# Performance work log

Measured on AMD Instinct MI355X. Metric: run time of the kernel, lower is better.

## Reference

```python
import jax, jax.numpy as jnp
import numpy as np

K = 50  # top-k causal instances (UC_MIL constructor)


def setup_inputs() -> dict:
    key = jax.random.key(0)
    k1, k2 = jax.random.split(key)
    X = jax.random.normal(k1, (8, 4096, 768), dtype=jnp.float32)
    # GCN layer weight: nn.Linear(768, 1, bias=False) -> weight shape (1, 768)
    W = jax.random.normal(k2, (1, 768), dtype=jnp.float32) * 0.02
    return {"X": X, "W": W}


def reference(X, W):
    # X: (B, N, D) bag of instance features; W: (1, D) GCN weight
    B, N, D = X.shape
    k = K

    # --- build_adjacency_matrix, batched ---
    Xc = X - X.mean(axis=1, keepdims=True)                      # center over instances
    cov = jnp.einsum('bnd,bmd->bnm', Xc, Xc)                    # (B, N, N)
    var = jnp.sqrt(jnp.sum(Xc * Xc, axis=-1, keepdims=True)) + 1e-6  # (B, N, 1)
    corr = cov / (var * jnp.swapaxes(var, 1, 2))                # var @ var.T
    A = jnp.abs(corr)
    dinv = jnp.sum(A, axis=-1) ** (-0.5)                        # (B, N)
    # D @ A @ D with diagonal D == row/col scaling (same math, no dense diag)
    A_norm = dinv[:, :, None] * A * dinv[:, None, :]

    # --- 1-layer GCN score: (A_norm @ (X W^T)).squeeze(-1) ---
    XW = jnp.einsum('bnd,d->bn', X, W[0])                       # (B, N)
    S = jnp.einsum('bnm,bm->bn', A_norm, XW)                    # (B, N)

    # --- top-k causal / non-causal split, vectorized over batch ---
    _, topk_idx = jax.lax.top_k(S, k)                           # (B, k)
    F_c = jnp.take_along_axis(X, topk_idx[:, :, None], axis=1)  # (B, k, D)

    # non-topk indices in ascending order (torch.arange(N)[mask] semantics)
    flag = jnp.zeros((B, N), dtype=jnp.int32)
    flag = flag.at[jnp.arange(B)[:, None], topk_idx].set(1)
    non_idx = jnp.argsort(flag, axis=1, stable=True)[:, : N - k]  # (B, N-k)
    F_nc = jnp.take_along_axis(X, non_idx[:, :, None], axis=1)    # (B, N-k, D)

    # NOTE: original code has a bug: topk_indices = torch.stack(F_i_c, 0),
    # i.e. the second output is the gathered features, not the indices.
    # We replicate that faithfully.
    return (S,
            F_c,
            F_c.mean(axis=1, keepdims=True),
            F_nc.mean(axis=1, keepdims=True))
```

## Files before the change

kernel.cpp:

```cpp
#include <hip/hip_runtime.h>
#include <stdint.h>

typedef unsigned short u16;
typedef short bf16x8 __attribute__((ext_vector_type(8)));
typedef float f32x4 __attribute__((ext_vector_type(4)));
typedef unsigned long long ull;

#define NB 8
#define NROW 4096
#define ND 768
#define NKB 24
#define NRB 32
#define KTILE 4096
#define NTRI 528
#define TOPK 50

#define CPART_OFF 0u
#define CSUM_OFF  786432u
#define MEAN_OFF  811008u
#define RV_OFF    835584u
#define XW_OFF    966656u
#define T_OFF     1097728u
#define U_OFF     1228800u
#define SMALL_TOTAL 1359872u
#define HI_OFF    ((size_t)SMALL_TOTAL)
#define LO_OFF    (HI_OFF + 50331648ull)
#define COV_OFF   (LO_OFF + 50331648ull)

static __device__ __forceinline__ u16 f2bf(float f) {
  uint32_t u = __float_as_uint(f);
  u += 0x7FFFu + ((u >> 16) & 1u);
  return (u16)(u >> 16);
}
static __device__ __forceinline__ float bf2f(u16 h) {
  return __uint_as_float(((uint32_t)h) << 16);
}

static __device__ __forceinline__ void gload_lds16(const char* g, char* l) {
  __builtin_amdgcn_global_load_lds(
      (const __attribute__((address_space(1))) uint32_t*)(const void*)g,
      (__attribute__((address_space(3))) uint32_t*)(void*)l, 16, 0, 0);
}

static __device__ __forceinline__ int tile_swz(int t) {
  return (t & 7) * 66 + (t >> 3);
}

__global__ __launch_bounds__(256)
void colsum1_kernel(const float* __restrict__ X, float* __restrict__ part) {
  const int nc = blockIdx.x;
  const int d  = threadIdx.x + blockIdx.y * 256;
  const int b  = blockIdx.z;
  const float* p = X + ((size_t)b * NROW + (size_t)nc * 128) * ND + d;
  float s = 0.f;
  for (int i = 0; i < 128; ++i) s += p[(size_t)i * ND];
  part[((size_t)b * 32 + nc) * ND + d] = s;
}

__global__ __launch_bounds__(256)
void colsum2_kernel(const float* __restrict__ part, float* __restrict__ csum,
                    float* __restrict__ mean) {
  const int d = threadIdx.x + blockIdx.x * 256;
  const int b = blockIdx.y;
  float s = 0.f;
  for (int i = 0; i < 32; ++i) s += part[((size_t)b * 32 + i) * ND + d];
  csum[(size_t)b * ND + d] = s;
  mean[(size_t)b * ND + d] = s * (1.0f / 4096.0f);
}

__global__ __launch_bounds__(128)
void rowstats_kernel(const float* __restrict__ X, const float* __restrict__ W,
                     const float* __restrict__ mean,
                     u16* __restrict__ hi, u16* __restrict__ lo,
                     float* __restrict__ rv, float* __restrict__ xw) {
  const int n  = blockIdx.x;
  const int gb = blockIdx.y;
  const int tid = threadIdx.x;
  const float* xr = X + ((size_t)gb * NROW + n) * ND;
  const float* mb = mean + (size_t)gb * ND;
  const int r = n & 127, rbk = n >> 7;
  float ssq = 0.f, sw = 0.f;
  if (tid < 96) {
    const int d0 = tid * 8;
    const float4 xa = *(const float4*)(xr + d0);
    const float4 xb = *(const float4*)(xr + d0 + 4);
    const float4 ma = *(const float4*)(mb + d0);
    const float4 mc = *(const float4*)(mb + d0 + 4);
    const float4 wa = *(const float4*)(W + d0);
    const float4 wb = *(const float4*)(W + d0 + 4);
    float x[8]  = {xa.x, xa.y, xa.z, xa.w, xb.x, xb.y, xb.z, xb.w};
    float mm[8] = {ma.x, ma.y, ma.z, ma.w, mc.x, mc.y, mc.z, mc.w};
    float ww[8] = {wa.x, wa.y, wa.z, wa.w, wb.x, wb.y, wb.z, wb.w};
    u16 hbits[8], lbits[8];
#pragma unroll
    for (int i = 0; i < 8; ++i) {
      float xc = x[i] - mm[i];
      ssq += xc * xc;
      sw  += x[i] * ww[i];
      u16 hb = f2bf(xc);
      float hf = bf2f(hb);
      u16 lb2 = f2bf(xc - hf);
      hbits[i] = hb; lbits[i] = lb2;
    }
    const int kb = d0 >> 5;
    const int kk = d0 & 31;
    const size_t tbyte = ((size_t)((gb * NRB + rbk) * NKB + kb)) * 8192
                       + (size_t)((r * 64 + kk * 2) ^ ((r & 7) << 4));
    uint4 hv, lv;
    hv.x = (uint32_t)hbits[0] | ((uint32_t)hbits[1] << 16);
    hv.y = (uint32_t)hbits[2] | ((uint32_t)hbits[3] << 16);
    hv.z = (uint32_t)hbits[4] | ((uint32_t)hbits[5] << 16);
    hv.w = (uint32_t)hbits[6] | ((uint32_t)hbits[7] << 16);
    lv.x = (uint32_t)lbits[0] | ((uint32_t)lbits[1] << 16);
    lv.y = (uint32_t)lbits[2] | ((uint32_t)lbits[3] << 16);
    lv.z = (uint32_t)lbits[4] | ((uint32_t)lbits[5] << 16);
    lv.w = (uint32_t)lbits[6] | ((uint32_t)lbits[7] << 16);
    *(uint4*)((char*)hi + tbyte) = hv;
    *(uint4*)((char*)lo + tbyte) = lv;
  }
#pragma unroll
  for (int m = 1; m < 64; m <<= 1) {
    ssq += __shfl_xor(ssq, m, 64);
    sw  += __shfl_xor(sw, m, 64);
  }
  __shared__ float sh[4];
  const int w = tid >> 6, lane = tid & 63;
  if (lane == 0) { sh[w * 2] = ssq; sh[w * 2 + 1] = sw; }
  __syncthreads();
  if (tid == 0) {
    float S = sh[0] + sh[2];
    float T = sh[1] + sh[3];
    const size_t i = (size_t)gb * NROW + n;
    rv[i] = 1.0f / (sqrtf(S) + 1e-6f);
    xw[i] = T;
  }
}

static __device__ __forceinline__ bf16x8 read_frag(const u16* sm, int r, int kbyte) {
  const int byte = (r * 64 + kbyte) ^ ((r & 7) << 4);
  return *(const bf16x8*)((const char*)sm + byte);
}

__global__ __launch_bounds__(256, 2)
void gemm_acc_kernel(const u16* __restrict__ hi, const u16* __restrict__ lo,
                     const float* __restrict__ coef, float* __restrict__ outacc,
                     float* __restrict__ covout) {
  const int gb = blockIdx.y;
  const int tsw = tile_swz(blockIdx.x);
  int trem = tsw;
  int rb = 0;
  while (trem >= NRB - rb) { trem -= NRB - rb; ++rb; }
  const int cb = rb + trem;

  __shared__ u16 sm[4 * KTILE];
  u16* aHi = sm;
  u16* bHi = sm + KTILE;
  u16* aLo = sm + 2 * KTILE;
  u16* bLo = sm + 3 * KTILE;

  const int tid = threadIdx.x;
  const int lane = tid & 63;
  const int wid = tid >> 6;
  const int wrow = wid >> 1, wcol = wid & 1;
  const int l15 = lane & 15, lg = lane >> 4;

  const char* hA = (const char*)(hi + (size_t)((gb * NRB + rb) * NKB) * KTILE);
  const char* hB = (const char*)(hi + (size_t)((gb * NRB + cb) * NKB) * KTILE);
  const char* lA = (const char*)(lo + (size_t)((gb * NRB + rb) * NKB) * KTILE);
  const char* lB = (const char*)(lo + (size_t)((gb * NRB + cb) * NKB) * KTILE);

  f32x4 acc[4][4];
#pragma unroll
  for (int i = 0; i < 4; ++i)
#pragma unroll
    for (int j = 0; j < 4; ++j) acc[i][j] = f32x4{0.f, 0.f, 0.f, 0.f};

  for (int kb = 0; kb < NKB; ++kb) {
    __syncthreads();
    const size_t kb8 = (size_t)kb * 8192;
#pragma unroll
    for (int it = 0; it < 2; ++it) {
      const int off = it * 4096 + tid * 16;
      gload_lds16(hA + kb8 + off, (char*)aHi + off);
      gload_lds16(hB + kb8 + off, (char*)bHi + off);
      gload_lds16(lA + kb8 + off, (char*)aLo + off);
      gload_lds16(lB + kb8 + off, (char*)bLo + off);
    }
    __syncthreads();

    bf16x8 ah[4], bh[4], al[4], bl[4];
#pragma unroll
    for (int i = 0; i < 4; ++i) {
      ah[i] = read_frag(aHi, wrow * 64 + i * 16 + l15, lg * 16);
      bh[i] = read_frag(bHi, wcol * 64 + i * 16 + l15, lg * 16);
      al[i] = read_frag(aLo, wrow * 64 + i * 16 + l15, lg * 16);
      bl[i] = read_frag(bLo, wcol * 64 + i * 16 + l15, lg * 16);
    }
#pragma unroll
    for (int mi = 0; mi < 4; ++mi)
#pragma unroll
      for (int ni = 0; ni < 4; ++ni) {
        acc[mi][ni] = __builtin_amdgcn_mfma_f32_16x16x32_bf16(ah[mi], bh[ni], acc[mi][ni], 0, 0, 0);
        acc[mi][ni] = __builtin_amdgcn_mfma_f32_16x16x32_bf16(ah[mi], bl[ni], acc[mi][ni], 0, 0, 0);
        acc[mi][ni] = __builtin_amdgcn_mfma_f32_16x16x32_bf16(al[mi], bh[ni], acc[mi][ni], 0, 0, 0);
      }
  }

  const float* cf = coef + (size_t)gb * NROW;
  float* oa = outacc + (size_t)gb * NROW;
  const int rbase = rb * 128 + wrow * 64;
  const int cbase = cb * 128 + wcol * 64;

  float* cv = covout + ((size_t)gb * NTRI + tsw) * 16384;
#pragma unroll
  for (int mi = 0; mi < 4; ++mi)
#pragma unroll
    for (int ni = 0; ni < 4; ++ni)
#pragma unroll
      for (int j = 0; j < 4; ++j)
        cv[(wrow * 64 + mi * 16 + lg * 4 + j) * 128 + wcol * 64 + ni * 16 + l15] =
            fabsf(acc[mi][ni][j]);

  float ccol[4];
#pragma unroll
  for (int ni = 0; ni < 4; ++ni) ccol[ni] = cf[cbase + ni * 16 + l15];

  float rs[4][4];
#pragma unroll
  for (int mi = 0; mi < 4; ++mi)
#pragma unroll
    for (int j = 0; j < 4; ++j) {
      float s = 0.f;
#pragma unroll
      for (int ni = 0; ni < 4; ++ni) s += fabsf(acc[mi][ni][j]) * ccol[ni];
      rs[mi][j] = s;
    }
#pragma unroll
  for (int m = 1; m < 16; m <<= 1)
#pragma unroll
    for (int mi = 0; mi < 4; ++mi)
#pragma unroll
      for (int j = 0; j < 4; ++j) rs[mi][j] += __shfl_xor(rs[mi][j], m, 64);
  if (l15 == 0) {
#pragma unroll
    for (int mi = 0; mi < 4; ++mi)
#pragma unroll
      for (int j = 0; j < 4; ++j)
        atomicAdd(&oa[rbase + mi * 16 + lg * 4 + j], rs[mi][j]);
  }

  if (rb != cb) {
    float crow[4][4];
#pragma unroll
    for (int mi = 0; mi < 4; ++mi)
#pragma unroll
      for (int j = 0; j < 4; ++j) crow[mi][j] = cf[rbase + mi * 16 + lg * 4 + j];
    float cs[4];
#pragma unroll
    for (int ni = 0; ni < 4; ++ni) {
      float s = 0.f;
#pragma unroll
      for (int mi = 0; mi < 4; ++mi)
#pragma unroll
        for (int j = 0; j < 4; ++j) s += fabsf(acc[mi][ni][j]) * crow[mi][j];
      cs[ni] = s;
    }
#pragma unroll
    for (int ni = 0; ni < 4; ++ni) {
      cs[ni] += __shfl_xor(cs[ni], 16, 64);
      cs[ni] += __shfl_xor(cs[ni], 32, 64);
    }
    if (lg == 0) {
#pragma unroll
      for (int ni = 0; ni < 4; ++ni)
        atomicAdd(&oa[cbase + ni * 16 + l15], cs[ni]);
    }
  }
}

__global__ __launch_bounds__(256, 2)
void upass_kernel(const float* __restrict__ cov, const float* __restrict__ tt,
                  const float* __restrict__ rv, const float* __restrict__ xw,
                  float* __restrict__ uacc) {
  const int gb = blockIdx.y;
  const int tsw = tile_swz(blockIdx.x);
  int trem = tsw;
  int rb = 0;
  while (trem >= NRB - rb) { trem -= NRB - rb; ++rb; }
  const int cb = rb + trem;

  const float* A = cov + ((size_t)gb * NTRI + tsw) * 16384;
  const size_t bo = (size_t)gb * NROW;

  __shared__ float wr[128];
  __shared__ float plds[128 * 33];
  __shared__ float csum_p[8][128];

  const int t = threadIdx.x;
  const int g = t >> 5;
  const int l = t & 31;

  if (t < 128) {
    const int row = rb * 128 + t;
    wr[t] = (1.0f / sqrtf(rv[bo + row] * tt[bo + row])) * xw[bo + row] * rv[bo + row];
  }
  float4 wc4;
  {
    const int col = cb * 128 + l * 4;
    const float4 r4 = *(const float4*)(rv + bo + col);
    const float4 t4 = *(const float4*)(tt + bo + col);
    const float4 x4 = *(const float4*)(xw + bo + col);
    wc4.x = (1.0f / sqrtf(r4.x * t4.x)) * x4.x * r4.x;
    wc4.y = (1.0f / sqrtf(r4.y * t4.y)) * x4.y * r4.y;
    wc4.z = (1.0f / sqrtf(r4.z * t4.z)) * x4.z * r4.z;
    wc4.w = (1.0f / sqrtf(r4.w * t4.w)) * x4.w * r4.w;
  }
  __syncthreads();

  float sc0 = 0.f, sc1 = 0.f, sc2 = 0.f, sc3 = 0.f;
#pragma unroll
  for (int i = 0; i < 16; ++i) {
    const int r = g + i * 8;
    const f32x4 v = __builtin_nontemporal_load((const f32x4*)(A + r * 128 + l * 4));
    plds[r * 33 + l] = v[0] * wc4.x + v[1] * wc4.y + v[2] * wc4.z + v[3] * wc4.w;
    const float wrr = wr[r];
    sc0 += v[0] * wrr; sc1 += v[1] * wrr; sc2 += v[2] * wrr; sc3 += v[3] * wrr;
  }
  csum_p[g][l * 4 + 0] = sc0;
  csum_p[g][l * 4 + 1] = sc1;
  csum_p[g][l * 4 + 2] = sc2;
  csum_p[g][l * 4 + 3] = sc3;
  __syncthreads();

  float* ua = uacc + bo;
  if (t < 128) {
    float rsum = 0.f;
#pragma unroll
    for (int i = 0; i < 32; ++i) rsum += plds[t * 33 + i];
    atomicAdd(&ua[rb * 128 + t], rsum);
    if (rb != cb) {
      float s = 0.f;
#pragma unroll
      for (int gg = 0; gg < 8; ++gg) s += csum_p[gg][t];
      atomicAdd(&ua[cb * 128 + t], s);
    }
  }
}

__global__ __launch_bounds__(1024)
void topk_kernel(const float* __restrict__ tt, const float* __restrict__ rv,
                 const float* __restrict__ u, const float* __restrict__ X,
                 const float* __restrict__ csum, float* __restrict__ S,
                 float* __restrict__ outFc, float* __restrict__ outC,
                 float* __restrict__ outNC) {
  const int b = blockIdx.x;
  __shared__ ull keys[NROW];
  __shared__ ull wred[16];
  __shared__ int selLds[TOPK];
  const int t = threadIdx.x;
  const int lane = t & 63, w = t >> 6;
  const size_t bo = (size_t)b * NROW;
#pragma unroll
  for (int j = 0; j < 4; ++j) {
    const int i = t + j * 1024;
    const float rvi = rv[bo + i];
    const float s = (1.0f / sqrtf(rvi * tt[bo + i])) * rvi * u[bo + i];
    S[bo + i] = s;
    uint32_t uu = __float_as_uint(s);
    uu = (uu & 0x80000000u) ? ~uu : (uu | 0x80000000u);
    keys[i] = ((ull)uu << 32) | (uint32_t)(4095 - i);
  }
  __syncthreads();
  for (int r = 0; r < TOPK; ++r) {
    ull m = keys[t];
    ull m2 = keys[t + 1024]; if (m2 > m) m = m2;
    m2 = keys[t + 2048]; if (m2 > m) m = m2;
    m2 = keys[t + 3072]; if (m2 > m) m = m2;
#pragma unroll
    for (int sh = 1; sh < 64; sh <<= 1) {
      ull o = __shfl_xor(m, sh, 64);
      if (o > m) m = o;
    }
    if (lane == 0) wred[w] = m;
    __syncthreads();
    if (w == 0) {
      ull mm = wred[lane & 15];
#pragma unroll
      for (int sh = 1; sh < 16; sh <<= 1) {
        ull o = __shfl_xor(mm, sh, 64);
        if (o > mm) mm = o;
      }
      if (lane == 0) {
        const int sel = 4095 - (int)(mm & 0xFFFFFFFFu);
        selLds[r] = sel;
        keys[sel] = 0ULL;
      }
    }
    __syncthreads();
  }

  if (t < ND) {
    float s = 0.f;
    for (int r = 0; r < TOPK; ++r) {
      const int row = selLds[r];
      const float v = X[(bo + row) * ND + t];
      outFc[((size_t)b * TOPK + r) * ND + t] = v;
      s += v;
    }
    outC[(size_t)b * ND + t]  = s * (1.0f / 50.0f);
    outNC[(size_t)b * ND + t] = (csum[(size_t)b * ND + t] - s) * (1.0f / 4046.0f);
  }
}

extern "C" void kernel_launch(void* const* d_in, const int* in_sizes, int n_in,
                              void* d_out, int out_size, void* d_ws, size_t ws_size,
                              hipStream_t stream) {
  const float* X = (const float*)d_in[0];
  const float* W = (const float*)d_in[1];
  float* out = (float*)d_out;
  char* ws = (char*)d_ws;

  float* cpart = (float*)(ws + CPART_OFF);
  float* csum  = (float*)(ws + CSUM_OFF);
  float* mean  = (float*)(ws + MEAN_OFF);
  float* rv    = (float*)(ws + RV_OFF);
  float* xw    = (float*)(ws + XW_OFF);
  float* tacc  = (float*)(ws + T_OFF);
  float* uacc  = (float*)(ws + U_OFF);
  u16* hi      = (u16*)(ws + HI_OFF);
  u16* lo      = (u16*)(ws + LO_OFF);
  float* cov   = (float*)(ws + COV_OFF);

  float* outS  = out;
  float* outFc = out + 32768;
  float* outMC = out + 339968;
  float* outMN = out + 346112;

  hipMemsetAsync(ws + T_OFF, 0, 262144, stream);

  colsum1_kernel<<<dim3(32, 3, NB), 256, 0, stream>>>(X, cpart);
  colsum2_kernel<<<dim3(3, NB), 256, 0, stream>>>(cpart, csum, mean);
  rowstats_kernel<<<dim3(NROW, NB), 128, 0, stream>>>(X, W, mean, hi, lo, rv, xw);
  gemm_acc_kernel<<<dim3(NTRI, NB), 256, 0, stream>>>(hi, lo, rv, tacc, cov);
  upass_kernel<<<dim3(NTRI, NB), 256, 0, stream>>>(cov, tacc, rv, xw, uacc);
  topk_kernel<<<NB, 1024, 0, stream>>>(tacc, rv, uacc, X, csum, outS, outFc, outMC, outMN);
}
```

Measured before the change: 463.6 us.

## Replace iterative argmax top-k with radix-select on packed keys

```diff
diff --git a/kernel.cpp b/kernel.cpp
--- a/kernel.cpp
+++ b/kernel.cpp
@@ -355,11 +355,18 @@
                  float* __restrict__ outNC) {
   const int b = blockIdx.x;
   __shared__ ull keys[NROW];
-  __shared__ ull wred[16];
+  __shared__ unsigned int hist[256];
+  __shared__ unsigned int wsum[4];
+  __shared__ ull spref;
+  __shared__ int sR, seld;
+  __shared__ int cnt;
+  __shared__ ull cand[TOPK];
   __shared__ int selLds[TOPK];
+
   const int t = threadIdx.x;
   const int lane = t & 63, w = t >> 6;
   const size_t bo = (size_t)b * NROW;
+
 #pragma unroll
   for (int j = 0; j < 4; ++j) {
     const int i = t + j * 1024;
@@ -370,34 +377,67 @@
     uu = (uu & 0x80000000u) ? ~uu : (uu | 0x80000000u);
     keys[i] = ((ull)uu << 32) | (uint32_t)(4095 - i);
   }
-  __syncthreads();
-  for (int r = 0; r < TOPK; ++r) {
-    ull m = keys[t];
-    ull m2 = keys[t + 1024]; if (m2 > m) m = m2;
-    m2 = keys[t + 2048]; if (m2 > m) m = m2;
-    m2 = keys[t + 3072]; if (m2 > m) m = m2;
-#pragma unroll
-    for (int sh = 1; sh < 64; sh <<= 1) {
-      ull o = __shfl_xor(m, sh, 64);
-      if (o > m) m = o;
-    }
-    if (lane == 0) wred[w] = m;
-    __syncthreads();
-    if (w == 0) {
-      ull mm = wred[lane & 15];
-#pragma unroll
-      for (int sh = 1; sh < 16; sh <<= 1) {
-        ull o = __shfl_xor(mm, sh, 64);
-        if (o > mm) mm = o;
+  if (t == 0) { spref = 0ULL; sR = TOPK; cnt = 0; }
+  __syncthreads();
+
+  for (int p = 7; p >= 0; --p) {
+    if (t < 256) hist[t] = 0u;
+    if (t == 0) seld = -1;
+    __syncthreads();
+    const ull pref = spref;
+    const ull mask = (p == 7) ? 0ULL : (~0ULL << ((p + 1) * 8));
+#pragma unroll
+    for (int j = 0; j < 4; ++j) {
+      const ull k = keys[t + j * 1024];
+      if ((k & mask) == pref)
+        atomicAdd(&hist[(unsigned int)(k >> (p * 8)) & 255u], 1u);
+    }
+    __syncthreads();
+    unsigned int sv = 0;
+    if (t < 256) {
+      sv = hist[t];
+#pragma unroll
+      for (int off = 1; off < 64; off <<= 1) {
+        unsigned int o = __shfl_down(sv, off, 64);
+        if (lane + off < 64) sv += o;
       }
-      if (lane == 0) {
-        const int sel = 4095 - (int)(mm & 0xFFFFFFFFu);
-        selLds[r] = sel;
-        keys[sel] = 0ULL;
-      }
-    }
-    __syncthreads();
-  }
+      if (lane == 0) wsum[w] = sv;
+    }
+    __syncthreads();
+    if (t < 256) {
+      unsigned int add = 0;
+#pragma unroll
+      for (int ww = 0; ww < 4; ++ww)
+        if (ww > w) add += wsum[ww];
+      sv += add;
+      if ((int)sv >= sR) atomicMax(&seld, t);
+    }
+    __syncthreads();
+    if (t == seld) {
+      sR = sR - (int)(sv - hist[t]);
+      spref = spref | ((ull)(unsigned int)t << (p * 8));
+    }
+    __syncthreads();
+  }
+  const ull kth = spref;
+
+#pragma unroll
+  for (int j = 0; j < 4; ++j) {
+    const ull k = keys[t + j * 1024];
+    if (k >= kth) {
+      const int ppos = atomicAdd(&cnt, 1);
+      cand[ppos] = k;
+    }
+  }
+  __syncthreads();
+  if (t < TOPK) {
+    const ull me = cand[t];
+    int r = 0;
+#pragma unroll 10
+    for (int i = 0; i < TOPK; ++i) r += (cand[i] > me);
+    selLds[r] = 4095 - (int)(me & 0xFFFFFFFFu);
+  }
+  __syncthreads();
 
   if (t < ND) {
     float s = 0.f;
```

New measurement: 431.4 us. 1.07x faster.
